# Optimization experiments

Hardware: AMD Instinct MI355X
Metric: run time of the kernel (lower is better)

## Reference

```python
import jax, jax.numpy as jnp
import numpy as np

BASE = 256
H = BASE * 2          # lstm_dim = 512
V = 32000             # out_dim
B, T = 16, 256


def setup_inputs() -> dict:
    key = jax.random.key(0)
    ks = jax.random.split(key, 12)
    s = 1.0 / np.sqrt(H)
    u = lambda k, shape: jax.random.uniform(k, shape, jnp.float32, -s, s)
    return {
        "words": jax.random.randint(ks[0], (B, T), 0, V),
        # tied embedding / output projection weight [V, H]
        "embed_W": jax.random.normal(ks[1], (V, H), jnp.float32),
        "fc_b": u(ks[2], (V,)),
        # LSTMCell 1: input 2H -> hidden H (torch gate order i,f,g,o)
        "w_ih1": u(ks[3], (4 * H, 2 * H)),
        "w_hh1": u(ks[4], (4 * H, H)),
        "b_ih1": u(ks[5], (4 * H,)),
        "b_hh1": u(ks[6], (4 * H,)),
        # LSTMCell 2: input H -> hidden H
        "w_ih2": u(ks[7], (4 * H, H)),
        "w_hh2": u(ks[8], (4 * H, H)),
        "b_ih2": u(ks[9], (4 * H,)),
        "b_hh2": u(ks[10], (4 * H,)),
    }


def _lstm_cell(x, h, c, w_ih, w_hh, b_ih, b_hh):
    gates = x @ w_ih.T + b_ih + h @ w_hh.T + b_hh  # [B, 4H]
    i, f, g, o = jnp.split(gates, 4, axis=-1)
    c = jax.nn.sigmoid(f) * c + jax.nn.sigmoid(i) * jnp.tanh(g)
    h = jax.nn.sigmoid(o) * jnp.tanh(c)
    return h, c


def reference(words, embed_W, fc_b, w_ih1, w_hh1, b_ih1, b_hh1,
              w_ih2, w_hh2, b_ih2, b_hh2):
    Bsz, Tlen = words.shape
    Hd = embed_W.shape[1]
    # The torch loop never updates `word`: it always embeds words[:, 0],
    # and context is always zeros. So the cell input is constant per step.
    x0 = embed_W[words[:, 0]]                                  # [B, H]
    x = jnp.concatenate([x0, jnp.zeros((Bsz, Hd), x0.dtype)], axis=1)  # [B, 2H]
    # first_step path == zero-initialized (h, c); dropout p=0.05 is identity in eval.
    z = jnp.zeros((Bsz, Hd), x0.dtype)

    def step(carry, _):
        h1, c1, h2, c2 = carry
        h1, c1 = _lstm_cell(x, h1, c1, w_ih1, w_hh1, b_ih1, b_hh1)
        h2, c2 = _lstm_cell(h1, h2, c2, w_ih2, w_hh2, b_ih2, b_hh2)
        return (h1, c1, h2, c2), h2

    _, h2_seq = jax.lax.scan(step, (z, z, z, z), None, length=Tlen - 1)  # [T-1, B, H]
    logits = jnp.einsum('tbh,vh->btv', h2_seq, embed_W) + fc_b           # [B, T-1, V]
    zeros0 = jnp.zeros((Bsz, 1, embed_W.shape[0]), logits.dtype)
    return jnp.concatenate([zeros0, logits], axis=1)                      # [B, T, V]
```

## Files before the change

### kernel.cpp

```cpp
#include <hip/hip_runtime.h>

typedef __attribute__((ext_vector_type(8))) short short8;
typedef __attribute__((ext_vector_type(4))) float f32x4;
typedef unsigned long long ull;

__device__ __forceinline__ unsigned short f2bf(float f){
  unsigned u = __float_as_uint(f);
  u += 0x7FFFu + ((u >> 16) & 1u);
  return (unsigned short)(u >> 16);
}
__device__ __forceinline__ float sigm(float x){ return 1.f / (1.f + expf(-x)); }
__device__ __forceinline__ int aldr(const int* p){
  return __hip_atomic_load(p, __ATOMIC_RELAXED, __HIP_MEMORY_SCOPE_AGENT);
}
__device__ __forceinline__ ull ald8(const ull* p){
  return __hip_atomic_load(p, __ATOMIC_RELAXED, __HIP_MEMORY_SCOPE_AGENT);
}
__device__ __forceinline__ void ast8(ull* p, ull v){
  __hip_atomic_store(p, v, __ATOMIC_RELAXED, __HIP_MEMORY_SCOPE_AGENT);
}
__device__ __forceinline__ void asti(int* p, int v){
  __hip_atomic_store(p, v, __ATOMIC_RELAXED, __HIP_MEMORY_SCOPE_AGENT);
}
__device__ __forceinline__ ull pack2b(float he, float ho, unsigned tag){
  unsigned lo = (unsigned)f2bf(he) | ((unsigned)f2bf(ho) << 16);
  return ((ull)tag << 32) | (ull)lo;
}
__device__ __forceinline__ short8 ld_bf16frag(const float* p){
  float4 x = *(const float4*)p, y = *(const float4*)(p + 4);
  short8 fr;
  fr[0]=(short)f2bf(x.x); fr[1]=(short)f2bf(x.y); fr[2]=(short)f2bf(x.z); fr[3]=(short)f2bf(x.w);
  fr[4]=(short)f2bf(y.x); fr[5]=(short)f2bf(y.y); fr[6]=(short)f2bf(y.z); fr[7]=(short)f2bf(y.w);
  return fr;
}


__global__ void k_embed_cvt(const float* __restrict__ e, unsigned short* __restrict__ ebf){
  long i = ((long)blockIdx.x * 256 + threadIdx.x) * 4;
  float4 v = *(const float4*)(e + i);
  ushort4 o;
  o.x = f2bf(v.x); o.y = f2bf(v.y); o.z = f2bf(v.z); o.w = f2bf(v.w);
  *(ushort4*)(ebf + i) = o;
}

__global__ void k_prep_misc(const float* __restrict__ b_ih2, const float* __restrict__ b_hh2,
                            float* __restrict__ b2c, ull* __restrict__ h1tag0,
                            ull* __restrict__ h2tag0, unsigned short* __restrict__ h2bf0,
                            int* __restrict__ done){
  int i = blockIdx.x * 256 + threadIdx.x;
  if(i < 4096){ h1tag0[i] = 0ull; h2tag0[i] = 0ull; }
  h2bf0[i] = 0;
  if(i < 2048){ b2c[i] = b_ih2[i] + b_hh2[i]; }
  if(i < 4096){ done[i] = 0; }
}

__global__ void k_a1const(const int* __restrict__ words, const float* __restrict__ embed,
                          const float* __restrict__ w_ih1, const float* __restrict__ b_ih1,
                          const float* __restrict__ b_hh1, float* __restrict__ a1c){
  int bb = threadIdx.x & 15, jj = threadIdx.x >> 4;
  int j = blockIdx.x * 16 + jj;
  const float* x0 = embed + (long)words[bb * 256] * 512;
  const float* wr = w_ih1 + (long)j * 1024;
  float acc = 0.f;
  for(int k = 0; k < 512; k += 4){
    float4 a = *(const float4*)(x0 + k);
    float4 b = *(const float4*)(wr + k);
    acc += a.x*b.x + a.y*b.y + a.z*b.z + a.w*b.w;
  }
  a1c[bb * 2048 + j] = acc + b_ih1[j] + b_hh1[j];
}

__global__ void __launch_bounds__(256, 1) k_recur(
    const float* __restrict__ w_hh1, const float* __restrict__ w_ih2, const float* __restrict__ w_hh2,
    const float* __restrict__ a1c, const float* __restrict__ b2c,
    ull* __restrict__ h1tag, ull* __restrict__ h2tag, unsigned short* __restrict__ h2bf,
    int* done){
  __shared__ unsigned A32[12288];
  unsigned short* A16 = (unsigned short*)A32;
  int* prog2 = done + 2048;
  const int bl = blockIdx.x, tid = threadIdx.x;
  const int l = tid & 63, w = tid >> 6;
  const int lu = l & 15, kq = l >> 4;
  const bool isL1 = (bl < 32);
  const int blk = isL1 ? bl : bl - 32;
  const int ubase = blk * 16;
  const int fu = tid & 15, fb = tid >> 4;
  float ag[4];
  float cst = 0.f;
  #pragma unroll
  for(int g = 0; g < 4; ++g)
    ag[g] = isL1 ? a1c[fb * 2048 + g * 512 + ubase + fu] : b2c[g * 512 + ubase + fu];

  if(isL1){
    float* prt = (float*)(A32 + 4096);
    short8 bw[4][4];
    #pragma unroll
    for(int n = 0; n < 4; ++n){
      const long wrow = (long)(n * 512 + ubase + lu);
      #pragma unroll
      for(int i = 0; i < 4; ++i){
        int kk = w * 128 + i * 32 + kq * 8;
        bw[n][i] = ld_bf16frag(w_hh1 + wrow * 512 + kk);
      }
    }
    for(int s = 1; s <= 255; ++s){
      if(((s & 15) == 1) && s > 48 && tid < 64){
        for(;;){
          int ok = (tid < 32) ? (aldr(prog2 + tid * 16) >= s - 40) : 1;
          if(__all(ok)) break;
          __builtin_amdgcn_s_sleep(1);
        }
      }
      {
        const ull* src = h1tag + ((s - 1) & 63) * 4096;
        const unsigned want = (unsigned)(s - 1);
        ull v[16];
        #pragma unroll
        for(int j = 0; j < 16; ++j) v[j] = ald8(src + tid + 256 * j);
        for(;;){
          bool bad = false;
          #pragma unroll
          for(int j = 0; j < 16; ++j)
            if((unsigned)(v[j] >> 32) != want){ v[j] = ald8(src + tid + 256 * j); bad = true; }
          if(!bad) break;
        }
        #pragma unroll
        for(int j = 0; j < 16; ++j){
          int wd = tid + 256 * j, b = wd >> 8, pr = wd & 255;
          A32[b * 256 + (((pr >> 2) ^ (b & 7)) << 2) + (pr & 3)] = (unsigned)v[j];
        }
      }
      __syncthreads();
      f32x4 acc[4] = {};
      #pragma unroll
      for(int i = 0; i < 4; ++i){
        int k8 = w * 16 + i * 4 + kq;
        const short8* ap = (const short8*)(A16 + lu * 512 + ((k8 ^ (lu & 7)) << 3));
        #pragma unroll
        for(int n = 0; n < 4; ++n)
          acc[n] = __builtin_amdgcn_mfma_f32_16x16x32_bf16(*ap, bw[n][i], acc[n], 0, 0, 0);
      }
      #pragma unroll
      for(int n = 0; n < 4; ++n)
        #pragma unroll
        for(int j = 0; j < 4; ++j)
          prt[w * 1024 + n * 256 + (kq * 4 + j) * 16 + lu] = acc[n][j];
      __syncthreads();
      {
        float g4[4];
        #pragma unroll
        for(int g = 0; g < 4; ++g){
          int c = g * 256 + fb * 16 + fu;
          g4[g] = ag[g] + prt[c] + prt[1024 + c] + prt[2048 + c] + prt[3072 + c];
        }
        cst = sigm(g4[1]) * cst + sigm(g4[0]) * tanhf(g4[2]);
        float h = sigm(g4[3]) * tanhf(cst);
        float hn = __shfl(h, tid + 1);
        if((fu & 1) == 0)
          ast8(h1tag + (s & 63) * 4096 + fb * 256 + blk * 8 + (fu >> 1), pack2b(h, hn, (unsigned)s));
      }
    }
  } else {
    float* prt = (float*)(A32 + 8192);
    short8 bw[4][8];
    #pragma unroll
    for(int n = 0; n < 4; ++n){
      const long wrow = (long)(n * 512 + ubase + lu);
      #pragma unroll
      for(int i = 0; i < 8; ++i){
        int kk = w * 256 + i * 32 + kq * 8;
        const float* p = (kk < 512) ? (w_ih2 + wrow * 512 + kk)
                                    : (w_hh2 + wrow * 512 + (kk - 512));
        bw[n][i] = ld_bf16frag(p);
      }
    }
    for(int s = 1; s <= 255; ++s){
      const ull* s1 = h1tag + (s & 63) * 4096;
      const ull* s2 = h2tag + ((s - 1) & 63) * 4096;
      const unsigned w1 = (unsigned)s, w2 = (unsigned)(s - 1);
      ull v1[16], v2[16];
      #pragma unroll
      for(int j = 0; j < 16; ++j) v1[j] = ald8(s1 + tid + 256 * j);
      #pragma unroll
      for(int j = 0; j < 16; ++j) v2[j] = ald8(s2 + tid + 256 * j);
      for(;;){
        bool bad = false;
        #pragma unroll
        for(int j = 0; j < 16; ++j)
          if((unsigned)(v1[j] >> 32) != w1){ v1[j] = ald8(s1 + tid + 256 * j); bad = true; }
        if(!bad) break;
      }
      for(;;){
        bool bad = false;
        #pragma unroll
        for(int j = 0; j < 16; ++j)
          if((unsigned)(v2[j] >> 32) != w2){ v2[j] = ald8(s2 + tid + 256 * j); bad = true; }
        if(!bad) break;
      }
      #pragma unroll
      for(int j = 0; j < 16; ++j){
        int wd = tid + 256 * j, b = wd >> 8, pr = wd & 255;
        int sw = (((pr >> 2) ^ (b & 7)) << 2) + (pr & 3);
        A32[b * 512 + sw] = (unsigned)v1[j];
        A32[b * 512 + 256 + sw] = (unsigned)v2[j];
      }
      __syncthreads();
      f32x4 acc[4] = {};
      #pragma unroll
      for(int i = 0; i < 8; ++i){
        int k8 = w * 32 + i * 4 + kq;
        const short8* ap = (const short8*)(A16 + lu * 1024 + ((k8 ^ (lu & 7)) << 3));
        #pragma unroll
        for(int n = 0; n < 4; ++n)
          acc[n] = __builtin_amdgcn_mfma_f32_16x16x32_bf16(*ap, bw[n][i], acc[n], 0, 0, 0);
      }
      #pragma unroll
      for(int n = 0; n < 4; ++n)
        #pragma unroll
        for(int j = 0; j < 4; ++j)
          prt[w * 1024 + n * 256 + (kq * 4 + j) * 16 + lu] = acc[n][j];
      __syncthreads();
      {
        float g4[4];
        #pragma unroll
        for(int g = 0; g < 4; ++g){
          int c = g * 256 + fb * 16 + fu;
          g4[g] = ag[g] + prt[c] + prt[1024 + c] + prt[2048 + c] + prt[3072 + c];
        }
        cst = sigm(g4[1]) * cst + sigm(g4[0]) * tanhf(g4[2]);
        float h = sigm(g4[3]) * tanhf(cst);
        float hn = __shfl(h, tid + 1);
        if((fu & 1) == 0)
          ast8(h2tag + (s & 63) * 4096 + fb * 256 + blk * 8 + (fu >> 1), pack2b(h, hn, (unsigned)s));
        h2bf[((long)s * 16 + fb) * 512 + ubase + fu] = f2bf(h);
      }
      if(tid == 0) asti(prog2 + blk * 16, s);
    }
  }
}

__global__ void __launch_bounds__(256, 2) k_proj(const unsigned short* __restrict__ A,
                                                 const unsigned short* __restrict__ Bm,
                                                 const float* __restrict__ fc_b,
                                                 float* __restrict__ out){
  __shared__ __align__(16) unsigned short As[4096];
  __shared__ __align__(16) unsigned short Bs[4096];
  const int tid = threadIdx.x;
  const int lane = tid & 63, w = tid >> 6;
  const int wr = w >> 1, wc = w & 1;
  const long mbase = (long)blockIdx.y * 128;
  const long nbase = (long)blockIdx.x * 128;
  f32x4 acc[4][4] = {};

  const int lrow = lane >> 2;
  const int lcol = (lane & 3) * 8;
  for(int kt = 0; kt < 16; ++kt){
    #pragma unroll
    for(int r = 0; r < 2; ++r){
      const unsigned short* ga = A  + (mbase + r*64 + w*16 + lrow) * 512 + kt*32 + lcol;
      __builtin_amdgcn_global_load_lds((const __attribute__((address_space(1))) void*)ga,
          (__attribute__((address_space(3))) void*)((char*)As + r*4096 + w*1024), 16, 0, 0);
      const unsigned short* gb = Bm + (nbase + r*64 + w*16 + lrow) * 512 + kt*32 + lcol;
      __builtin_amdgcn_global_load_lds((const __attribute__((address_space(1))) void*)gb,
          (__attribute__((address_space(3))) void*)((char*)Bs + r*4096 + w*1024), 16, 0, 0);
    }
    __syncthreads();
    short8 af[4], bf[4];
    const int kro = (lane >> 4) * 8;
    #pragma unroll
    for(int m = 0; m < 4; ++m){
      af[m] = *(const short8*)(As + (wr*64 + m*16 + (lane & 15)) * 32 + kro);
      bf[m] = *(const short8*)(Bs + (wc*64 + m*16 + (lane & 15)) * 32 + kro);
    }
    #pragma unroll
    for(int m = 0; m < 4; ++m){
      #pragma unroll
      for(int n = 0; n < 4; ++n){
        acc[m][n] = __builtin_amdgcn_mfma_f32_16x16x32_bf16(af[m], bf[n], acc[m][n], 0, 0, 0);
      }
    }
    __syncthreads();
  }
  const int crow0 = (lane >> 4) * 4;
  const int ccol = lane & 15;
  float fb[4];
  #pragma unroll
  for(int n = 0; n < 4; ++n) fb[n] = fc_b[nbase + wc*64 + n*16 + ccol];
  #pragma unroll
  for(int m = 0; m < 4; ++m){
    #pragma unroll
    for(int j = 0; j < 4; ++j){
      long rr = mbase + wr*64 + m*16 + crow0 + j;
      int t = (int)(rr >> 4), b = (int)(rr & 15);
      float* orow = out + ((long)b * 256 + t) * 32000;
      #pragma unroll
      for(int n = 0; n < 4; ++n){
        float v = (t == 0) ? 0.f : (acc[m][n][j] + fb[n]);
        orow[nbase + wc*64 + n*16 + ccol] = v;
      }
    }
  }
}

extern "C" void kernel_launch(void* const* d_in, const int* in_sizes, int n_in,
                              void* d_out, int out_size, void* d_ws, size_t ws_size,
                              hipStream_t stream){
  const int*   words = (const int*)  d_in[0];
  const float* embed = (const float*)d_in[1];
  const float* fc_b  = (const float*)d_in[2];
  const float* w_ih1 = (const float*)d_in[3];
  const float* w_hh1 = (const float*)d_in[4];
  const float* b_ih1 = (const float*)d_in[5];
  const float* b_hh1 = (const float*)d_in[6];
  const float* w_ih2 = (const float*)d_in[7];
  const float* w_hh2 = (const float*)d_in[8];
  const float* b_ih2 = (const float*)d_in[9];
  const float* b_hh2 = (const float*)d_in[10];
  float* out = (float*)d_out;
  char* ws = (char*)d_ws;

  unsigned short* embed_bf = (unsigned short*)(ws + 0);
  unsigned short* h2bf     = (unsigned short*)(ws + 32768000);
  ull* h1tag = (ull*)(ws + 36962304);
  ull* h2tag = (ull*)(ws + 39059456);
  float* a1c = (float*)(ws + 41156608);
  float* b2c = (float*)(ws + 41287680);
  int*   done = (int*) (ws + 41295872);

  k_embed_cvt<<<16000, 256, 0, stream>>>(embed, embed_bf);
  k_prep_misc<<<32, 256, 0, stream>>>(b_ih2, b_hh2, b2c, h1tag, h2tag, h2bf, done);
  k_a1const<<<128, 256, 0, stream>>>(words, embed, w_ih1, b_ih1, b_hh1, a1c);

  void* args[9];
  args[0] = (void*)&w_hh1; args[1] = (void*)&w_ih2; args[2] = (void*)&w_hh2;
  args[3] = (void*)&a1c;   args[4] = (void*)&b2c;
  args[5] = (void*)&h1tag; args[6] = (void*)&h2tag; args[7] = (void*)&h2bf;
  args[8] = (void*)&done;
  hipError_t ce = hipLaunchCooperativeKernel((const void*)k_recur, dim3(64), dim3(256),
                                             args, 0, stream);
  if(ce != hipSuccess){
    k_recur<<<dim3(64), dim3(256), 0, stream>>>(w_hh1, w_ih2, w_hh2, a1c, b2c,
                                                h1tag, h2tag, h2bf, done);
  }

  k_proj<<<dim3(250, 32), 256, 0, stream>>>(h2bf, embed_bf, fc_b, out);
}
```

Before: 1.131 ms.

## Fuse output projection into persistent recurrence kernel with progress-gated work stealing

Removes the separate projection GEMM launch and runs it inside the cooperative recurrence kernel. The grid grows to 256 blocks: the 64 recurrence blocks join the pool once their time steps finish, and 192 extra blocks pull 128x128 output tiles from an atomic counter. Each worker waits until layer-2 progress flags cover the tile's time rows, so the projection overlaps with the sequential LSTM instead of running after it. The cost is extra contention on the CUs while the latency-bound recurrence runs, plus spin waits. h2 is now written as bf16 pairs with atomic stores and a block barrier before the progress flag is published, so projection blocks see complete rows.

```diff
diff --git a/kernel.cpp b/kernel.cpp
--- a/kernel.cpp
+++ b/kernel.cpp
@@ -70,14 +70,100 @@
   a1c[bb * 2048 + j] = acc + b_ih1[j] + b_hh1[j];
 }
 
+__device__ __forceinline__ void proj_worker(unsigned* A32, const unsigned short* Ah,
+    const unsigned short* Bm, const float* __restrict__ fc_b, float* __restrict__ out,
+    int* prog2, int* ctr, int tid){
+  unsigned short* As = (unsigned short*)A32;
+  unsigned short* Bs = (unsigned short*)A32 + 4096;
+  int* sbox = (int*)(A32 + 4096);
+  const int lane = tid & 63, w = tid >> 6;
+  const int wr = w >> 1, wc = w & 1;
+  const int lrow = lane >> 2;
+  const int lcol = (lane & 3) * 8;
+  int curgate = -1;
+  for(;;){
+    if(tid == 0)
+      *sbox = __hip_atomic_fetch_add(ctr, 1, __ATOMIC_RELAXED, __HIP_MEMORY_SCOPE_AGENT);
+    __syncthreads();
+    int tix = *sbox;
+    __syncthreads();
+    if(tix >= 8000) break;
+    int mb = tix / 250, nb = tix - mb * 250;
+    int tEnd = mb * 8 + 7;
+    if(tEnd > curgate){
+      if(tid < 64){
+        for(;;){
+          int ok = (tid < 32) ? (aldr(prog2 + tid * 16) >= tEnd) : 1;
+          if(__all(ok)) break;
+          __builtin_amdgcn_s_sleep(1);
+        }
+        __builtin_amdgcn_fence(__ATOMIC_ACQUIRE, "agent");
+      }
+      __syncthreads();
+      curgate = tEnd;
+    }
+    const long mbase = (long)mb * 128;
+    const long nbase = (long)nb * 128;
+    f32x4 acc[4][4] = {};
+    for(int kt = 0; kt < 16; ++kt){
+      #pragma unroll
+      for(int r = 0; r < 2; ++r){
+        const unsigned short* ga = Ah + (mbase + r*64 + w*16 + lrow) * 512 + kt*32 + lcol;
+        __builtin_amdgcn_global_load_lds((const __attribute__((address_space(1))) void*)ga,
+            (__attribute__((address_space(3))) void*)((char*)As + r*4096 + w*1024), 16, 0, 0);
+        const unsigned short* gb = Bm + (nbase + r*64 + w*16 + lrow) * 512 + kt*32 + lcol;
+        __builtin_amdgcn_global_load_lds((const __attribute__((address_space(1))) void*)gb,
+            (__attribute__((address_space(3))) void*)((char*)Bs + r*4096 + w*1024), 16, 0, 0);
+      }
+      __syncthreads();
+      short8 af[4], bf[4];
+      const int kro = (lane >> 4) * 8;
+      #pragma unroll
+      for(int m = 0; m < 4; ++m){
+        af[m] = *(const short8*)(As + (wr*64 + m*16 + (lane & 15)) * 32 + kro);
+        bf[m] = *(const short8*)(Bs + (wc*64 + m*16 + (lane & 15)) * 32 + kro);
+      }
+      #pragma unroll
+      for(int m = 0; m < 4; ++m){
+        #pragma unroll
+        for(int n = 0; n < 4; ++n){
+          acc[m][n] = __builtin_amdgcn_mfma_f32_16x16x32_bf16(af[m], bf[n], acc[m][n], 0, 0, 0);
+        }
+      }
+      __syncthreads();
+    }
+    const int crow0 = (lane >> 4) * 4;
+    const int ccol = lane & 15;
+    float fb4[4];
+    #pragma unroll
+    for(int n = 0; n < 4; ++n) fb4[n] = fc_b[nbase + wc*64 + n*16 + ccol];
+    #pragma unroll
+    for(int m = 0; m < 4; ++m){
+      #pragma unroll
+      for(int j = 0; j < 4; ++j){
+        long rr = mbase + wr*64 + m*16 + crow0 + j;
+        int t = (int)(rr >> 4), b = (int)(rr & 15);
+        float* orow = out + ((long)b * 256 + t) * 32000;
+        #pragma unroll
+        for(int n = 0; n < 4; ++n){
+          float v = (t == 0) ? 0.f : (acc[m][n][j] + fb4[n]);
+          orow[nbase + wc*64 + n*16 + ccol] = v;
+        }
+      }
+    }
+  }
+}
+
 __global__ void __launch_bounds__(256, 1) k_recur(
     const float* __restrict__ w_hh1, const float* __restrict__ w_ih2, const float* __restrict__ w_hh2,
     const float* __restrict__ a1c, const float* __restrict__ b2c,
     ull* __restrict__ h1tag, ull* __restrict__ h2tag, unsigned short* __restrict__ h2bf,
-    int* done){
+    int* done, const unsigned short* __restrict__ embed_bf,
+    const float* __restrict__ fc_b, float* __restrict__ out){
   __shared__ unsigned A32[12288];
   unsigned short* A16 = (unsigned short*)A32;
   int* prog2 = done + 2048;
+  int* ctr   = done + 1600;
   const int bl = blockIdx.x, tid = threadIdx.x;
   const int l = tid & 63, w = tid >> 6;
   const int lu = l & 15, kq = l >> 4;
@@ -85,221 +171,166 @@
   const int blk = isL1 ? bl : bl - 32;
   const int ubase = blk * 16;
   const int fu = tid & 15, fb = tid >> 4;
-  float ag[4];
-  float cst = 0.f;
-  #pragma unroll
-  for(int g = 0; g < 4; ++g)
-    ag[g] = isL1 ? a1c[fb * 2048 + g * 512 + ubase + fu] : b2c[g * 512 + ubase + fu];
-
-  if(isL1){
-    float* prt = (float*)(A32 + 4096);
-    short8 bw[4][4];
+
+  if(bl < 64){
+    float ag[4];
+    float cst = 0.f;
     #pragma unroll
-    for(int n = 0; n < 4; ++n){
-      const long wrow = (long)(n * 512 + ubase + lu);
-      #pragma unroll
-      for(int i = 0; i < 4; ++i){
-        int kk = w * 128 + i * 32 + kq * 8;
-        bw[n][i] = ld_bf16frag(w_hh1 + wrow * 512 + kk);
-      }
-    }
-    for(int s = 1; s <= 255; ++s){
-      if(((s & 15) == 1) && s > 48 && tid < 64){
-        for(;;){
-          int ok = (tid < 32) ? (aldr(prog2 + tid * 16) >= s - 40) : 1;
-          if(__all(ok)) break;
-          __builtin_amdgcn_s_sleep(1);
-        }
-      }
-      {
-        const ull* src = h1tag + ((s - 1) & 63) * 4096;
-        const unsigned want = (unsigned)(s - 1);
-        ull v[16];
-        #pragma unroll
-        for(int j = 0; j < 16; ++j) v[j] = ald8(src + tid + 256 * j);
+    for(int g = 0; g < 4; ++g)
+      ag[g] = isL1 ? a1c[fb * 2048 + g * 512 + ubase + fu] : b2c[g * 512 + ubase + fu];
+
+    if(isL1){
+      float* prt = (float*)(A32 + 4096);
+      short8 bw[4][4];
+      #pragma unroll
+      for(int n = 0; n < 4; ++n){
+        const long wrow = (long)(n * 512 + ubase + lu);
+        #pragma unroll
+        for(int i = 0; i < 4; ++i){
+          int kk = w * 128 + i * 32 + kq * 8;
+          bw[n][i] = ld_bf16frag(w_hh1 + wrow * 512 + kk);
+        }
+      }
+      for(int s = 1; s <= 255; ++s){
+        if(((s & 15) == 1) && s > 48 && tid < 64){
+          for(;;){
+            int ok = (tid < 32) ? (aldr(prog2 + tid * 16) >= s - 40) : 1;
+            if(__all(ok)) break;
+            __builtin_amdgcn_s_sleep(1);
+          }
+        }
+        {
+          const ull* src = h1tag + ((s - 1) & 63) * 4096;
+          const unsigned want = (unsigned)(s - 1);
+          ull v[16];
+          #pragma unroll
+          for(int j = 0; j < 16; ++j) v[j] = ald8(src + tid + 256 * j);
+          for(;;){
+            bool bad = false;
+            #pragma unroll
+            for(int j = 0; j < 16; ++j)
+              if((unsigned)(v[j] >> 32) != want){ v[j] = ald8(src + tid + 256 * j); bad = true; }
+            if(!bad) break;
+          }
+          #pragma unroll
+          for(int j = 0; j < 16; ++j){
+            int wd = tid + 256 * j, b = wd >> 8, pr = wd & 255;
+            A32[b * 256 + (((pr >> 2) ^ (b & 7)) << 2) + (pr & 3)] = (unsigned)v[j];
+          }
+        }
+        __syncthreads();
+        f32x4 acc[4] = {};
+        #pragma unroll
+        for(int i = 0; i < 4; ++i){
+          int k8 = w * 16 + i * 4 + kq;
+          const short8* ap = (const short8*)(A16 + lu * 512 + ((k8 ^ (lu & 7)) << 3));
+          #pragma unroll
+          for(int n = 0; n < 4; ++n)
+            acc[n] = __builtin_amdgcn_mfma_f32_16x16x32_bf16(*ap, bw[n][i], acc[n], 0, 0, 0);
+        }
+        #pragma unroll
+        for(int n = 0; n < 4; ++n)
+          #pragma unroll
+          for(int j = 0; j < 4; ++j)
+            prt[w * 1024 + n * 256 + (kq * 4 + j) * 16 + lu] = acc[n][j];
+        __syncthreads();
+        {
+          float g4[4];
+          #pragma unroll
+          for(int g = 0; g < 4; ++g){
+            int c = g * 256 + fb * 16 + fu;
+            g4[g] = ag[g] + prt[c] + prt[1024 + c] + prt[2048 + c] + prt[3072 + c];
+          }
+          cst = sigm(g4[1]) * cst + sigm(g4[0]) * tanhf(g4[2]);
+          float h = sigm(g4[3]) * tanhf(cst);
+          float hn = __shfl(h, tid + 1);
+          if((fu & 1) == 0)
+            ast8(h1tag + (s & 63) * 4096 + fb * 256 + blk * 8 + (fu >> 1), pack2b(h, hn, (unsigned)s));
+        }
+      }
+    } else {
+      float* prt = (float*)(A32 + 8192);
+      short8 bw[4][8];
+      #pragma unroll
+      for(int n = 0; n < 4; ++n){
+        const long wrow = (long)(n * 512 + ubase + lu);
+        #pragma unroll
+        for(int i = 0; i < 8; ++i){
+          int kk = w * 256 + i * 32 + kq * 8;
+          const float* p = (kk < 512) ? (w_ih2 + wrow * 512 + kk)
+                                      : (w_hh2 + wrow * 512 + (kk - 512));
+          bw[n][i] = ld_bf16frag(p);
+        }
+      }
+      for(int s = 1; s <= 255; ++s){
+        const ull* s1 = h1tag + (s & 63) * 4096;
+        const ull* s2 = h2tag + ((s - 1) & 63) * 4096;
+        const unsigned w1 = (unsigned)s, w2 = (unsigned)(s - 1);
+        ull v1[16], v2[16];
+        #pragma unroll
+        for(int j = 0; j < 16; ++j) v1[j] = ald8(s1 + tid + 256 * j);
+        #pragma unroll
+        for(int j = 0; j < 16; ++j) v2[j] = ald8(s2 + tid + 256 * j);
         for(;;){
           bool bad = false;
           #pragma unroll
           for(int j = 0; j < 16; ++j)
-            if((unsigned)(v[j] >> 32) != want){ v[j] = ald8(src + tid + 256 * j); bad = true; }
+            if((unsigned)(v1[j] >> 32) != w1){ v1[j] = ald8(s1 + tid + 256 * j); bad = true; }
+          if(!bad) break;
+        }
+        for(;;){
+          bool bad = false;
+          #pragma unroll
+          for(int j = 0; j < 16; ++j)
+            if((unsigned)(v2[j] >> 32) != w2){ v2[j] = ald8(s2 + tid + 256 * j); bad = true; }
           if(!bad) break;
         }
         #pragma unroll
         for(int j = 0; j < 16; ++j){
           int wd = tid + 256 * j, b = wd >> 8, pr = wd & 255;
-          A32[b * 256 + (((pr >> 2) ^ (b & 7)) << 2) + (pr & 3)] = (unsigned)v[j];
-        }
-      }
-      __syncthreads();
-      f32x4 acc[4] = {};
-      #pragma unroll
-      for(int i = 0; i < 4; ++i){
-        int k8 = w * 16 + i * 4 + kq;
-        const short8* ap = (const short8*)(A16 + lu * 512 + ((k8 ^ (lu & 7)) << 3));
+          int sw = (((pr >> 2) ^ (b & 7)) << 2) + (pr & 3);
+          A32[b * 512 + sw] = (unsigned)v1[j];
+          A32[b * 512 + 256 + sw] = (unsigned)v2[j];
+        }
+        __syncthreads();
+        f32x4 acc[4] = {};
+        #pragma unroll
+        for(int i = 0; i < 8; ++i){
+          int k8 = w * 32 + i * 4 + kq;
+          const short8* ap = (const short8*)(A16 + lu * 1024 + ((k8 ^ (lu & 7)) << 3));
+          #pragma unroll
+          for(int n = 0; n < 4; ++n)
+            acc[n] = __builtin_amdgcn_mfma_f32_16x16x32_bf16(*ap, bw[n][i], acc[n], 0, 0, 0);
+        }
         #pragma unroll
         for(int n = 0; n < 4; ++n)
-          acc[n] = __builtin_amdgcn_mfma_f32_16x16x32_bf16(*ap, bw[n][i], acc[n], 0, 0, 0);
-      }
-      #pragma unroll
-      for(int n = 0; n < 4; ++n)
-        #pragma unroll
-        for(int j = 0; j < 4; ++j)
-          prt[w * 1024 + n * 256 + (kq * 4 + j) * 16 + lu] = acc[n][j];
-      __syncthreads();
-      {
-        float g4[4];
-        #pragma unroll
-        for(int g = 0; g < 4; ++g){
-          int c = g * 256 + fb * 16 + fu;
-          g4[g] = ag[g] + prt[c] + prt[1024 + c] + prt[2048 + c] + prt[3072 + c];
-        }
-        cst = sigm(g4[1]) * cst + sigm(g4[0]) * tanhf(g4[2]);
-        float h = sigm(g4[3]) * tanhf(cst);
-        float hn = __shfl(h, tid + 1);
-        if((fu & 1) == 0)
-          ast8(h1tag + (s & 63) * 4096 + fb * 256 + blk * 8 + (fu >> 1), pack2b(h, hn, (unsigned)s));
-      }
-    }
-  } else {
-    float* prt = (float*)(A32 + 8192);
-    short8 bw[4][8];
-    #pragma unroll
-    for(int n = 0; n < 4; ++n){
-      const long wrow = (long)(n * 512 + ubase + lu);
-      #pragma unroll
-      for(int i = 0; i < 8; ++i){
-        int kk = w * 256 + i * 32 + kq * 8;
-        const float* p = (kk < 512) ? (w_ih2 + wrow * 512 + kk)
-                                    : (w_hh2 + wrow * 512 + (kk - 512));
-        bw[n][i] = ld_bf16frag(p);
-      }
-    }
-    for(int s = 1; s <= 255; ++s){
-      const ull* s1 = h1tag + (s & 63) * 4096;
-      const ull* s2 = h2tag + ((s - 1) & 63) * 4096;
-      const unsigned w1 = (unsigned)s, w2 = (unsigned)(s - 1);
-      ull v1[16], v2[16];
-      #pragma unroll
-      for(int j = 0; j < 16; ++j) v1[j] = ald8(s1 + tid + 256 * j);
-      #pragma unroll
-      for(int j = 0; j < 16; ++j) v2[j] = ald8(s2 + tid + 256 * j);
-      for(;;){
-        bool bad = false;
-        #pragma unroll
-        for(int j = 0; j < 16; ++j)
-          if((unsigned)(v1[j] >> 32) != w1){ v1[j] = ald8(s1 + tid + 256 * j); bad = true; }
-        if(!bad) break;
-      }
-      for(;;){
-        bool bad = false;
-        #pragma unroll
-        for(int j = 0; j < 16; ++j)
-          if((unsigned)(v2[j] >> 32) != w2){ v2[j] = ald8(s2 + tid + 256 * j); bad = true; }
-        if(!bad) break;
-      }
-      #pragma unroll
-      for(int j = 0; j < 16; ++j){
-        int wd = tid + 256 * j, b = wd >> 8, pr = wd & 255;
-        int sw = (((pr >> 2) ^ (b & 7)) << 2) + (pr & 3);
-        A32[b * 512 + sw] = (unsigned)v1[j];
-        A32[b * 512 + 256 + sw] = (unsigned)v2[j];
-      }
-      __syncthreads();
-      f32x4 acc[4] = {};
-      #pragma unroll
-      for(int i = 0; i < 8; ++i){
-        int k8 = w * 32 + i * 4 + kq;
-        const short8* ap = (const short8*)(A16 + lu * 1024 + ((k8 ^ (lu & 7)) << 3));
-        #pragma unroll
-        for(int n = 0; n < 4; ++n)
-          acc[n] = __builtin_amdgcn_mfma_f32_16x16x32_bf16(*ap, bw[n][i], acc[n], 0, 0, 0);
-      }
-      #pragma unroll
-      for(int n = 0; n < 4; ++n)
-        #pragma unroll
-        for(int j = 0; j < 4; ++j)
-          prt[w * 1024 + n * 256 + (kq * 4 + j) * 16 + lu] = acc[n][j];
-      __syncthreads();
-      {
-        float g4[4];
-        #pragma unroll
-        for(int g = 0; g < 4; ++g){
-          int c = g * 256 + fb * 16 + fu;
-          g4[g] = ag[g] + prt[c] + prt[1024 + c] + prt[2048 + c] + prt[3072 + c];
-        }
-        cst = sigm(g4[1]) * cst + sigm(g4[0]) * tanhf(g4[2]);
-        float h = sigm(g4[3]) * tanhf(cst);
-        float hn = __shfl(h, tid + 1);
-        if((fu & 1) == 0)
-          ast8(h2tag + (s & 63) * 4096 + fb * 256 + blk * 8 + (fu >> 1), pack2b(h, hn, (unsigned)s));
-        h2bf[((long)s * 16 + fb) * 512 + ubase + fu] = f2bf(h);
-      }
-      if(tid == 0) asti(prog2 + blk * 16, s);
+          #pragma unroll
+          for(int j = 0; j < 4; ++j)
+            prt[w * 1024 + n * 256 + (kq * 4 + j) * 16 + lu] = acc[n][j];
+        __syncthreads();
+        {
+          float g4[4];
+          #pragma unroll
+          for(int g = 0; g < 4; ++g){
+            int c = g * 256 + fb * 16 + fu;
+            g4[g] = ag[g] + prt[c] + prt[1024 + c] + prt[2048 + c] + prt[3072 + c];
+          }
+          cst = sigm(g4[1]) * cst + sigm(g4[0]) * tanhf(g4[2]);
+          float h = sigm(g4[3]) * tanhf(cst);
+          float hn = __shfl(h, tid + 1);
+          if((fu & 1) == 0){
+            ast8(h2tag + (s & 63) * 4096 + fb * 256 + blk * 8 + (fu >> 1), pack2b(h, hn, (unsigned)s));
+            asti((int*)(h2bf + ((long)s * 16 + fb) * 512 + ubase + fu),
+                 (int)((unsigned)f2bf(h) | ((unsigned)f2bf(hn) << 16)));
+          }
+        }
+        __syncthreads();
+        if(tid == 0) asti(prog2 + blk * 16, s);
+      }
     }
   }
-}
-
-__global__ void __launch_bounds__(256, 2) k_proj(const unsigned short* __restrict__ A,
-                                                 const unsigned short* __restrict__ Bm,
-                                                 const float* __restrict__ fc_b,
-                                                 float* __restrict__ out){
-  __shared__ __align__(16) unsigned short As[4096];
-  __shared__ __align__(16) unsigned short Bs[4096];
-  const int tid = threadIdx.x;
-  const int lane = tid & 63, w = tid >> 6;
-  const int wr = w >> 1, wc = w & 1;
-  const long mbase = (long)blockIdx.y * 128;
-  const long nbase = (long)blockIdx.x * 128;
-  f32x4 acc[4][4] = {};
-
-  const int lrow = lane >> 2;
-  const int lcol = (lane & 3) * 8;
-  for(int kt = 0; kt < 16; ++kt){
-    #pragma unroll
-    for(int r = 0; r < 2; ++r){
-      const unsigned short* ga = A  + (mbase + r*64 + w*16 + lrow) * 512 + kt*32 + lcol;
-      __builtin_amdgcn_global_load_lds((const __attribute__((address_space(1))) void*)ga,
-          (__attribute__((address_space(3))) void*)((char*)As + r*4096 + w*1024), 16, 0, 0);
-      const unsigned short* gb = Bm + (nbase + r*64 + w*16 + lrow) * 512 + kt*32 + lcol;
-      __builtin_amdgcn_global_load_lds((const __attribute__((address_space(1))) void*)gb,
-          (__attribute__((address_space(3))) void*)((char*)Bs + r*4096 + w*1024), 16, 0, 0);
-    }
-    __syncthreads();
-    short8 af[4], bf[4];
-    const int kro = (lane >> 4) * 8;
-    #pragma unroll
-    for(int m = 0; m < 4; ++m){
-      af[m] = *(const short8*)(As + (wr*64 + m*16 + (lane & 15)) * 32 + kro);
-      bf[m] = *(const short8*)(Bs + (wc*64 + m*16 + (lane & 15)) * 32 + kro);
-    }
-    #pragma unroll
-    for(int m = 0; m < 4; ++m){
-      #pragma unroll
-      for(int n = 0; n < 4; ++n){
-        acc[m][n] = __builtin_amdgcn_mfma_f32_16x16x32_bf16(af[m], bf[n], acc[m][n], 0, 0, 0);
-      }
-    }
-    __syncthreads();
-  }
-  const int crow0 = (lane >> 4) * 4;
-  const int ccol = lane & 15;
-  float fb[4];
-  #pragma unroll
-  for(int n = 0; n < 4; ++n) fb[n] = fc_b[nbase + wc*64 + n*16 + ccol];
-  #pragma unroll
-  for(int m = 0; m < 4; ++m){
-    #pragma unroll
-    for(int j = 0; j < 4; ++j){
-      long rr = mbase + wr*64 + m*16 + crow0 + j;
-      int t = (int)(rr >> 4), b = (int)(rr & 15);
-      float* orow = out + ((long)b * 256 + t) * 32000;
-      #pragma unroll
-      for(int n = 0; n < 4; ++n){
-        float v = (t == 0) ? 0.f : (acc[m][n][j] + fb[n]);
-        orow[nbase + wc*64 + n*16 + ccol] = v;
-      }
-    }
-  }
+
+  proj_worker(A32, h2bf, embed_bf, fc_b, out, prog2, ctr, tid);
 }
 
 extern "C" void kernel_launch(void* const* d_in, const int* in_sizes, int n_in,
@@ -331,17 +362,17 @@
   k_prep_misc<<<32, 256, 0, stream>>>(b_ih2, b_hh2, b2c, h1tag, h2tag, h2bf, done);
   k_a1const<<<128, 256, 0, stream>>>(words, embed, w_ih1, b_ih1, b_hh1, a1c);
 
-  void* args[9];
+  void* args[12];
   args[0] = (void*)&w_hh1; args[1] = (void*)&w_ih2; args[2] = (void*)&w_hh2;
   args[3] = (void*)&a1c;   args[4] = (void*)&b2c;
   args[5] = (void*)&h1tag; args[6] = (void*)&h2tag; args[7] = (void*)&h2bf;
-  args[8] = (void*)&done;
-  hipError_t ce = hipLaunchCooperativeKernel((const void*)k_recur, dim3(64), dim3(256),
+  args[8] = (void*)&done;  args[9] = (void*)&embed_bf;
+  args[10] = (void*)&fc_b; args[11] = (void*)&out;
+  hipError_t ce = hipLaunchCooperativeKernel((const void*)k_recur, dim3(256), dim3(256),
                                              args, 0, stream);
   if(ce != hipSuccess){
-    k_recur<<<dim3(64), dim3(256), 0, stream>>>(w_hh1, w_ih2, w_hh2, a1c, b2c,
-                                                h1tag, h2tag, h2bf, done);
+    k_recur<<<dim3(256), dim3(256), 0, stream>>>(w_hh1, w_ih2, w_hh2, a1c, b2c,
+                                                 h1tag, h2tag, h2bf, done,
+                                                 embed_bf, fc_b, out);
   }
-
-  k_proj<<<dim3(250, 32), 256, 0, stream>>>(h2bf, embed_bf, fc_b, out);
-}
+}
```

Result: faster. 968.0 us (-14.4%).
